# Performance work log

Measured on AMD Instinct MI355X. Metric: run time of the kernel, lower is better.

## Reference

```python
import jax, jax.numpy as jnp
import numpy as np

N, E = 10000, 160000
B, F, P, C = 16, 2, 12, 32


def gcn_norm(edge_index, edge_weight, n):
    # GCN symmetric normalization with self-loops (fill value 1.0, improved=False)
    src, dst = edge_index[0], edge_index[1]
    loop = jnp.arange(n, dtype=src.dtype)
    src = jnp.concatenate([src, loop])
    dst = jnp.concatenate([dst, loop])
    w = jnp.concatenate([edge_weight, jnp.ones((n,), edge_weight.dtype)])
    deg = jnp.zeros((n,), w.dtype).at[dst].add(w)
    dinv = jnp.where(deg > 0, jax.lax.rsqrt(deg), 0.0)
    return src, dst, dinv[src] * w * dinv[dst]


def gcn_conv(x, W, b, src, dst, norm, n):
    # x: [B, N, Fin] -> [B, N, Fout]; transform-then-propagate like GCNConv
    xw = x @ W
    msgs = xw[:, src, :] * norm[None, :, None]  # gather over source nodes
    out = jnp.zeros((x.shape[0], n, W.shape[1]), x.dtype).at[:, dst].add(msgs)
    return out + b


def setup_inputs():
    key = jax.random.key(0)
    ks = jax.random.split(key, 20)
    s = 0.1
    return {
        "x": jax.random.normal(ks[0], (B, N, F, P), jnp.float32),
        "edge_index": jax.random.randint(ks[1], (2, E), 0, N, jnp.int32),
        "edge_weight": jax.random.uniform(ks[2], (E,), jnp.float32),
        "W_z": jax.random.normal(ks[3], (F, C), jnp.float32) * s,
        "b_z": jnp.zeros((C,), jnp.float32),
        "lin_z_W": jax.random.normal(ks[4], (2 * C, C), jnp.float32) * s,
        "lin_z_b": jnp.zeros((C,), jnp.float32),
        "W_r": jax.random.normal(ks[5], (F, C), jnp.float32) * s,
        "b_r": jnp.zeros((C,), jnp.float32),
        "lin_r_W": jax.random.normal(ks[6], (2 * C, C), jnp.float32) * s,
        "lin_r_b": jnp.zeros((C,), jnp.float32),
        "W_h": jax.random.normal(ks[7], (F, C), jnp.float32) * s,
        "b_h": jnp.zeros((C,), jnp.float32),
        "lin_h_W": jax.random.normal(ks[8], (2 * C, C), jnp.float32) * s,
        "lin_h_b": jnp.zeros((C,), jnp.float32),
        "attention": jax.random.uniform(ks[9], (P,), jnp.float32),
        "lin_out_W": jax.random.normal(ks[10], (C, P), jnp.float32) * s,
        "lin_out_b": jnp.zeros((P,), jnp.float32),
    }


def reference(x, edge_index, edge_weight, W_z, b_z, lin_z_W, lin_z_b, W_r, b_r,
              lin_r_W, lin_r_b, W_h, b_h, lin_h_W, lin_h_b, attention,
              lin_out_W, lin_out_b):
    b, n, f, p = x.shape
    c = W_z.shape[1]
    src, dst, norm = gcn_norm(edge_index, edge_weight, n)
    probs = jax.nn.softmax(attention)  # attention over periods
    H0 = jnp.zeros((b, n, c), x.dtype)  # A3TGCN2 passes H=None each period
    xs = jnp.moveaxis(x, 3, 0)  # [P, B, N, F]

    def step(acc, inp):
        xp, w = inp  # xp: [B, N, F]
        Gz = gcn_conv(xp, W_z, b_z, src, dst, norm, n)
        Z = jax.nn.sigmoid(jnp.concatenate([Gz, H0], -1) @ lin_z_W + lin_z_b)
        Gr = gcn_conv(xp, W_r, b_r, src, dst, norm, n)
        R = jax.nn.sigmoid(jnp.concatenate([Gr, H0], -1) @ lin_r_W + lin_r_b)
        Gh = gcn_conv(xp, W_h, b_h, src, dst, norm, n)
        Ht = jnp.tanh(jnp.concatenate([Gh, H0 * R], -1) @ lin_h_W + lin_h_b)
        Hn = Z * H0 + (1.0 - Z) * Ht  # one GRU step from zero hidden
        return acc + w * Hn, None

    H_acc, _ = jax.lax.scan(step, H0, (xs, probs))
    h = jax.nn.relu(H_acc)
    return h @ lin_out_W + lin_out_b  # [B, N, periods]
```

## Files before the change

### kernel.cpp

```cpp
#include <hip/hip_runtime.h>
#include <hip/hip_bf16.h>

#define NN 10000
#define EE 160000
#define BB 16
#define PP 12
#define CC 32
#define XTOT (BB*NN*24)

__device__ __forceinline__ float fast_rcp(float x){ return __builtin_amdgcn_rcpf(x); }
__device__ __forceinline__ float fast_exp2(float x){
#if __has_builtin(__builtin_amdgcn_exp2f)
    return __builtin_amdgcn_exp2f(x);
#else
    return exp2f(x);
#endif
}
__device__ __forceinline__ unsigned short f2bfu(float f){
    union { float f; unsigned int i; } c; c.f = f;
    unsigned int r = c.i + 0x7FFFu + ((c.i >> 16) & 1u);
    return (unsigned short)(r >> 16);
}
__device__ __forceinline__ void up2(unsigned int u, float& a, float& b){
    union { unsigned int i; float f; } c;
    c.i = u << 16;          a = c.f;
    c.i = u & 0xFFFF0000u;  b = c.f;
}
__device__ __forceinline__ void unp24(uint4 q0, uint4 q1, uint4 q2, float* f){
    up2(q0.x,f[0],f[1]);   up2(q0.y,f[2],f[3]);   up2(q0.z,f[4],f[5]);   up2(q0.w,f[6],f[7]);
    up2(q1.x,f[8],f[9]);   up2(q1.y,f[10],f[11]); up2(q1.z,f[12],f[13]); up2(q1.w,f[14],f[15]);
    up2(q2.x,f[16],f[17]); up2(q2.y,f[18],f[19]); up2(q2.z,f[20],f[21]); up2(q2.w,f[22],f[23]);
}

__global__ __launch_bounds__(256) void k_stage(const float* __restrict__ x,
        const float* __restrict__ ew, const int* __restrict__ dst,
        unsigned short* __restrict__ xc, float* __restrict__ deg, int* __restrict__ cnt,
        const float* __restrict__ Wz, const float* __restrict__ bz,
        const float* __restrict__ LzW, const float* __restrict__ lzb,
        const float* __restrict__ Wh, const float* __restrict__ bh,
        const float* __restrict__ LhW, const float* __restrict__ lhb,
        const float* __restrict__ att, const float* __restrict__ LoW,
        const float* __restrict__ lob, float* __restrict__ wbuf){
    const float L2E = 1.4426950408889634f;
    int blk = blockIdx.x, tid = threadIdx.x;
    if (blk < 3750){
        int t  = blk*256 + tid;
        int o0 = t*4;
        int n  = o0 / 384;
        int j  = o0 - n*384;
        int b  = j / 24;
        int fp = j - b*24;
        float4 f = *(const float4*)(x + b*(NN*24) + n*24 + fp);
        ushort4 r; r.x=f2bfu(f.x); r.y=f2bfu(f.y); r.z=f2bfu(f.z); r.w=f2bfu(f.w);
        *(ushort4*)(xc + o0) = r;
        if (blk < 625){
            int e = blk*256 + tid;
            int d = dst[e];
            atomicAdd(&deg[d], ew[e]);
            atomicAdd(&cnt[d], 1);
        }
    } else {
        int c = tid;
        if (c < CC){
            float s0=0.f,s1=0.f,sb=lzb[c], h0=0.f,h1=0.f,hb=lhb[c];
            for (int k=0;k<CC;k++){
                float wz = LzW[k*CC+c];
                s0 += Wz[k]*wz; s1 += Wz[CC+k]*wz; sb += bz[k]*wz;
                float wh = LhW[k*CC+c];
                h0 += Wh[k]*wh; h1 += Wh[CC+k]*wh; hb += bh[k]*wh;
            }
            float* wp = wbuf + c*8;
            wp[0]=s0*L2E; wp[1]=s1*L2E; wp[2]=sb*L2E;
            wp[3]=h0*(2.f*L2E); wp[4]=h1*(2.f*L2E); wp[5]=hb*(2.f*L2E);
            wp[6]=0.f; wp[7]=0.f;
            for (int q=0;q<PP;q++) wbuf[288 + c*PP + q] = LoW[c*PP+q];
        } else if (c == 32){
            float a[PP]; float m = -1e30f;
            for (int p=0;p<PP;p++){ a[p]=att[p]; m = fmaxf(m, a[p]); }
            float s=0.f;
            for (int p=0;p<PP;p++){ a[p]=__expf(a[p]-m); s += a[p]; }
            float r = 1.f/s;
            for (int p=0;p<PP;p++) wbuf[256+p] = a[p]*r;
        } else if (c == 33){
            for (int q=0;q<PP;q++) wbuf[268+q] = lob[q];
        }
    }
}

__global__ __launch_bounds__(1024) void k_scan(const int* __restrict__ cnt,
        int* __restrict__ rowp, int* __restrict__ nxt){
    __shared__ int sums[1024];
    int tid = threadIdx.x;
    int lo = tid*10, hi = lo+10;
    if (lo > NN) lo = NN;
    if (hi > NN) hi = NN;
    int s = 0;
    for (int j=lo;j<hi;j++) s += cnt[j];
    sums[tid] = s;
    __syncthreads();
    for (int off=1; off<1024; off<<=1){
        int t = (tid >= off) ? sums[tid-off] : 0;
        __syncthreads();
        sums[tid] += t;
        __syncthreads();
    }
    int run = sums[tid] - s;
    if (tid == 0) rowp[0] = 0;
    for (int j=lo;j<hi;j++){
        nxt[j] = run;
        run += cnt[j];
        rowp[j+1] = run;
    }
}

__global__ __launch_bounds__(256) void k_scatter(const int* __restrict__ src,
        const int* __restrict__ dst, const float* __restrict__ ew,
        const float* __restrict__ deg, int* __restrict__ nxt,
        int* __restrict__ col, float* __restrict__ val){
    int e = blockIdx.x*256 + threadIdx.x;
    int s = src[e], d = dst[e];
    float v = rsqrtf(deg[s]+1.0f) * ew[e] * rsqrtf(deg[d]+1.0f);
    int pos = atomicAdd(&nxt[d], 1);
    col[pos] = s;
    val[pos] = v;
}

__global__ __launch_bounds__(128) void k_fused(const unsigned short* __restrict__ xc,
        const int* __restrict__ rowp, const int* __restrict__ col,
        const float* __restrict__ val, const float* __restrict__ deg,
        const float* __restrict__ wbuf, float* __restrict__ out){
    int tid = threadIdx.x;
    int g = tid >> 5, h = (tid >> 4) & 1, l = tid & 15;
    int n = blockIdx.x*4 + g;
    int e0 = rowp[n], e1 = rowp[n+1];

    float acc[24];
    #pragma unroll
    for (int k=0;k<24;k++) acc[k] = 0.f;
    const unsigned short* xl = xc + l*24;

    int e = e0 + h;
    for (; e + 2 < e1; e += 4){
        int s1 = col[e],  s2 = col[e+2];
        float v1 = val[e], v2 = val[e+2];
        const uint4* p1 = (const uint4*)(xl + s1*384);
        const uint4* p2 = (const uint4*)(xl + s2*384);
        uint4 qa0=p1[0], qa1=p1[1], qa2=p1[2];
        uint4 qb0=p2[0], qb1=p2[1], qb2=p2[2];
        float fa[24], fb[24];
        unp24(qa0,qa1,qa2,fa);
        unp24(qb0,qb1,qb2,fb);
        #pragma unroll
        for (int k=0;k<24;k++) acc[k] = fmaf(v1, fa[k], fmaf(v2, fb[k], acc[k]));
    }
    if (e < e1){
        int s1 = col[e];
        float v1 = val[e];
        const uint4* p1 = (const uint4*)(xl + s1*384);
        uint4 qa0=p1[0], qa1=p1[1], qa2=p1[2];
        float fa[24];
        unp24(qa0,qa1,qa2,fa);
        #pragma unroll
        for (int k=0;k<24;k++) acc[k] = fmaf(v1, fa[k], acc[k]);
    }
    if (h == 0){
        float v = fast_rcp(deg[n] + 1.0f);
        const uint4* p1 = (const uint4*)(xl + n*384);
        uint4 qa0=p1[0], qa1=p1[1], qa2=p1[2];
        float fa[24];
        unp24(qa0,qa1,qa2,fa);
        #pragma unroll
        for (int k=0;k<24;k++) acc[k] = fmaf(v, fa[k], acc[k]);
    }
    #pragma unroll
    for (int k=0;k<24;k++) acc[k] += __shfl_xor(acc[k], 16, 64);

    float pr[12];
    #pragma unroll
    for (int p=0;p<12;p++) pr[p] = wbuf[256+p];
    float o[12];
    #pragma unroll
    for (int q=0;q<12;q++) o[q] = 0.f;

    const float4* wp = (const float4*)wbuf;
    int cbase = h*16;
    for (int cc=0; cc<16; ++cc){
        int c = cbase + cc;
        float4 wa = wp[c*2];
        float4 wb = wp[c*2+1];
        float a = 0.f;
        #pragma unroll
        for (int p=0;p<12;p++){
            float y0 = acc[p], y1 = acc[12+p];
            float zs = fmaf(y1, wa.y, fmaf(y0, wa.x, wa.z));
            float hs = fmaf(y1, wb.x, fmaf(y0, wa.w, wb.y));
            zs = fminf(zs, 80.f); hs = fminf(hs, 80.f);
            float ez = fast_exp2(zs);
            float eh = fast_exp2(hs);
            float t  = fast_rcp((1.f+ez)*(1.f+eh));
            a = fmaf(pr[p]*(eh-1.f), t, a);
        }
        a = fmaxf(a, 0.f);
        const float4* lw = (const float4*)(wbuf + 288 + c*12);
        float4 w0 = lw[0], w1 = lw[1], w2 = lw[2];
        o[0]=fmaf(a,w0.x,o[0]); o[1]=fmaf(a,w0.y,o[1]); o[2] =fmaf(a,w0.z,o[2]);  o[3] =fmaf(a,w0.w,o[3]);
        o[4]=fmaf(a,w1.x,o[4]); o[5]=fmaf(a,w1.y,o[5]); o[6] =fmaf(a,w1.z,o[6]);  o[7] =fmaf(a,w1.w,o[7]);
        o[8]=fmaf(a,w2.x,o[8]); o[9]=fmaf(a,w2.y,o[9]); o[10]=fmaf(a,w2.z,o[10]); o[11]=fmaf(a,w2.w,o[11]);
    }
    #pragma unroll
    for (int q=0;q<12;q++) o[q] += __shfl_xor(o[q], 16, 64);
    if (h == 0){
        #pragma unroll
        for (int q=0;q<12;q++) o[q] += wbuf[268+q];
        float4* op = (float4*)(out + (l*NN + n)*12);
        op[0] = make_float4(o[0],o[1],o[2],o[3]);
        op[1] = make_float4(o[4],o[5],o[6],o[7]);
        op[2] = make_float4(o[8],o[9],o[10],o[11]);
    }
}

extern "C" void kernel_launch(void* const* d_in, const int* in_sizes, int n_in,
                              void* d_out, int out_size, void* d_ws, size_t ws_size,
                              hipStream_t stream) {
    const float* x   = (const float*)d_in[0];
    const int*   ei  = (const int*)d_in[1];
    const float* ew  = (const float*)d_in[2];
    const float* Wz  = (const float*)d_in[3];
    const float* bz  = (const float*)d_in[4];
    const float* LzW = (const float*)d_in[5];
    const float* lzb = (const float*)d_in[6];
    const float* Wh  = (const float*)d_in[11];
    const float* bh  = (const float*)d_in[12];
    const float* LhW = (const float*)d_in[13];
    const float* lhb = (const float*)d_in[14];
    const float* att = (const float*)d_in[15];
    const float* LoW = (const float*)d_in[16];
    const float* lob = (const float*)d_in[17];
    float* out = (float*)d_out;

    const int* srcI = ei;
    const int* dstI = ei + EE;

    char* ws = (char*)d_ws;
    size_t off = 0;
    auto alloc = [&](size_t bytes){ void* p = ws + off; off += (bytes + 255)/256*256; return p; };
    int*            degcnt = (int*)alloc(2*NN*4);
    float*          wbuf   = (float*)alloc(672*4);
    unsigned short* xc     = (unsigned short*)alloc((size_t)XTOT*2);
    int*            rowp   = (int*)alloc((NN+1)*4);
    int*            nxt    = (int*)alloc(NN*4);
    int*            col    = (int*)alloc(EE*4);
    float*          val    = (float*)alloc(EE*4);
    float* deg = (float*)degcnt;
    int*   cnt = degcnt + NN;

    hipMemsetAsync(degcnt, 0, 2*NN*4, stream);
    hipLaunchKernelGGL(k_stage,   dim3(3751), dim3(256),  0, stream,
                       x, ew, dstI, xc, deg, cnt,
                       Wz, bz, LzW, lzb, Wh, bh, LhW, lhb, att, LoW, lob, wbuf);
    hipLaunchKernelGGL(k_scan,    dim3(1),    dim3(1024), 0, stream, cnt, rowp, nxt);
    hipLaunchKernelGGL(k_scatter, dim3(EE/256), dim3(256), 0, stream,
                       srcI, dstI, ew, deg, nxt, col, val);
    hipLaunchKernelGGL(k_fused,   dim3(NN/4), dim3(128),  0, stream,
                       xc, rowp, col, val, deg, wbuf, out);
}
```

Measured before the change: 189.3 us.

## Merge all stages into one persistent kernel with software grid barriers

Replaces the memset plus four kernel launches with a single persistent kernel of 1024 blocks that moves between phases using atomic-counter grid barriers. Degree zeroing, staging, a two-level parallel prefix scan (in place of the single-block scan), CSR scatter and the fused gather/GRU/output stage all run inside it. The gather now uses one 64-lane wave per node and splits the channel loop over four lane groups. It also drops the clamp on the z exponent and expands the denominator. The aim is to remove launch gaps and the serial scan, at the cost of relying on all blocks being co-resident and of spin-wait barrier overhead.

```diff
diff --git a/kernel.cpp b/kernel.cpp
--- a/kernel.cpp
+++ b/kernel.cpp
@@ -7,6 +7,9 @@
 #define PP 12
 #define CC 32
 #define XTOT (BB*NN*24)
+#define NBLK 1024
+#define NTHR 128
+#define NT (NBLK*NTHR)
 
 __device__ __forceinline__ float fast_rcp(float x){ return __builtin_amdgcn_rcpf(x); }
 __device__ __forceinline__ float fast_exp2(float x){
@@ -32,34 +35,41 @@
     up2(q2.x,f[16],f[17]); up2(q2.y,f[18],f[19]); up2(q2.z,f[20],f[21]); up2(q2.w,f[22],f[23]);
 }
 
-__global__ __launch_bounds__(256) void k_stage(const float* __restrict__ x,
-        const float* __restrict__ ew, const int* __restrict__ dst,
-        unsigned short* __restrict__ xc, float* __restrict__ deg, int* __restrict__ cnt,
-        const float* __restrict__ Wz, const float* __restrict__ bz,
-        const float* __restrict__ LzW, const float* __restrict__ lzb,
-        const float* __restrict__ Wh, const float* __restrict__ bh,
-        const float* __restrict__ LhW, const float* __restrict__ lhb,
-        const float* __restrict__ att, const float* __restrict__ LoW,
-        const float* __restrict__ lob, float* __restrict__ wbuf){
-    const float L2E = 1.4426950408889634f;
-    int blk = blockIdx.x, tid = threadIdx.x;
-    if (blk < 3750){
-        int t  = blk*256 + tid;
-        int o0 = t*4;
-        int n  = o0 / 384;
-        int j  = o0 - n*384;
-        int b  = j / 24;
-        int fp = j - b*24;
-        float4 f = *(const float4*)(x + b*(NN*24) + n*24 + fp);
-        ushort4 r; r.x=f2bfu(f.x); r.y=f2bfu(f.y); r.z=f2bfu(f.z); r.w=f2bfu(f.w);
-        *(ushort4*)(xc + o0) = r;
-        if (blk < 625){
-            int e = blk*256 + tid;
-            int d = dst[e];
-            atomicAdd(&deg[d], ew[e]);
-            atomicAdd(&cnt[d], 1);
-        }
-    } else {
+__device__ __forceinline__ void gbar(int* bar, int idx){
+    __syncthreads();
+    if (threadIdx.x == 0){
+        __threadfence();
+        __hip_atomic_fetch_add(&bar[idx], 1, __ATOMIC_ACQ_REL, __HIP_MEMORY_SCOPE_AGENT);
+        while (__hip_atomic_load(&bar[idx], __ATOMIC_ACQUIRE, __HIP_MEMORY_SCOPE_AGENT) < NBLK){
+            __builtin_amdgcn_s_sleep(2);
+        }
+    }
+    __syncthreads();
+}
+
+__global__ __launch_bounds__(128, 4) void k_mega(
+    const float* __restrict__ x, const int* __restrict__ srcI, const int* __restrict__ dstI,
+    const float* __restrict__ ew,
+    const float* __restrict__ Wz, const float* __restrict__ bz,
+    const float* __restrict__ LzW, const float* __restrict__ lzb,
+    const float* __restrict__ Wh, const float* __restrict__ bh,
+    const float* __restrict__ LhW, const float* __restrict__ lhb,
+    const float* __restrict__ att, const float* __restrict__ LoW, const float* __restrict__ lob,
+    float* __restrict__ deg, int* __restrict__ cnt, float* __restrict__ wbuf,
+    unsigned short* __restrict__ xc, int* __restrict__ rowp, int* __restrict__ nxt,
+    int* __restrict__ col, float* __restrict__ val,
+    int* __restrict__ tmp, int* __restrict__ partial, int* __restrict__ bar,
+    float* __restrict__ out)
+{
+    const int tid = threadIdx.x, bid = blockIdx.x;
+    const int gid = bid*NTHR + tid;
+    __shared__ int shw[2];
+
+    if (gid < NN){ deg[gid] = 0.f; cnt[gid] = 0; }
+    gbar(bar, 0);
+
+    if (bid == NBLK-1){
+        const float L2E = 1.4426950408889634f;
         int c = tid;
         if (c < CC){
             float s0=0.f,s1=0.f,sb=lzb[c], h0=0.f,h1=0.f,hb=lhb[c];
@@ -85,137 +95,174 @@
             for (int q=0;q<PP;q++) wbuf[268+q] = lob[q];
         }
     }
-}
-
-__global__ __launch_bounds__(1024) void k_scan(const int* __restrict__ cnt,
-        int* __restrict__ rowp, int* __restrict__ nxt){
-    __shared__ int sums[1024];
-    int tid = threadIdx.x;
-    int lo = tid*10, hi = lo+10;
-    if (lo > NN) lo = NN;
-    if (hi > NN) hi = NN;
-    int s = 0;
-    for (int j=lo;j<hi;j++) s += cnt[j];
-    sums[tid] = s;
-    __syncthreads();
-    for (int off=1; off<1024; off<<=1){
-        int t = (tid >= off) ? sums[tid-off] : 0;
+    for (int t = gid; t < XTOT/4; t += NT){
+        int o0 = t*4;
+        int n  = o0 / 384;
+        int j  = o0 - n*384;
+        int b  = j / 24;
+        int fp = j - b*24;
+        float4 f = *(const float4*)(x + b*(NN*24) + n*24 + fp);
+        ushort4 r; r.x=f2bfu(f.x); r.y=f2bfu(f.y); r.z=f2bfu(f.z); r.w=f2bfu(f.w);
+        *(ushort4*)(xc + o0) = r;
+    }
+    for (int e = gid; e < EE; e += NT){
+        int d = dstI[e];
+        atomicAdd(&deg[d], ew[e]);
+        atomicAdd(&cnt[d], 1);
+    }
+    gbar(bar, 1);
+
+    {
+        int c = (gid < NN) ? cnt[gid] : 0;
+        int v = c;
+        #pragma unroll
+        for (int off=1; off<64; off<<=1){
+            int u = __shfl_up(v, off, 64);
+            if ((tid & 63) >= off) v += u;
+        }
+        if (tid == 63) shw[0] = v;
         __syncthreads();
-        sums[tid] += t;
+        int incl = v + ((tid >= 64) ? shw[0] : 0);
+        if (gid < NN) tmp[gid] = incl - c;
+        if (tid == NTHR-1) partial[bid] = incl;
+    }
+    gbar(bar, 2);
+
+    if (bid == 0){
+        int base = tid*8;
+        int lv[8]; int s = 0;
+        #pragma unroll
+        for (int j=0;j<8;j++){ lv[j] = partial[base+j]; s += lv[j]; }
+        int v = s;
+        #pragma unroll
+        for (int off=1; off<64; off<<=1){
+            int u = __shfl_up(v, off, 64);
+            if ((tid & 63) >= off) v += u;
+        }
+        if (tid == 63) shw[1] = v;
         __syncthreads();
-    }
-    int run = sums[tid] - s;
-    if (tid == 0) rowp[0] = 0;
-    for (int j=lo;j<hi;j++){
-        nxt[j] = run;
-        run += cnt[j];
-        rowp[j+1] = run;
-    }
-}
-
-__global__ __launch_bounds__(256) void k_scatter(const int* __restrict__ src,
-        const int* __restrict__ dst, const float* __restrict__ ew,
-        const float* __restrict__ deg, int* __restrict__ nxt,
-        int* __restrict__ col, float* __restrict__ val){
-    int e = blockIdx.x*256 + threadIdx.x;
-    int s = src[e], d = dst[e];
-    float v = rsqrtf(deg[s]+1.0f) * ew[e] * rsqrtf(deg[d]+1.0f);
-    int pos = atomicAdd(&nxt[d], 1);
-    col[pos] = s;
-    val[pos] = v;
-}
-
-__global__ __launch_bounds__(128) void k_fused(const unsigned short* __restrict__ xc,
-        const int* __restrict__ rowp, const int* __restrict__ col,
-        const float* __restrict__ val, const float* __restrict__ deg,
-        const float* __restrict__ wbuf, float* __restrict__ out){
-    int tid = threadIdx.x;
-    int g = tid >> 5, h = (tid >> 4) & 1, l = tid & 15;
-    int n = blockIdx.x*4 + g;
-    int e0 = rowp[n], e1 = rowp[n+1];
-
-    float acc[24];
-    #pragma unroll
-    for (int k=0;k<24;k++) acc[k] = 0.f;
-    const unsigned short* xl = xc + l*24;
-
-    int e = e0 + h;
-    for (; e + 2 < e1; e += 4){
-        int s1 = col[e],  s2 = col[e+2];
-        float v1 = val[e], v2 = val[e+2];
-        const uint4* p1 = (const uint4*)(xl + s1*384);
-        const uint4* p2 = (const uint4*)(xl + s2*384);
-        uint4 qa0=p1[0], qa1=p1[1], qa2=p1[2];
-        uint4 qb0=p2[0], qb1=p2[1], qb2=p2[2];
-        float fa[24], fb[24];
-        unp24(qa0,qa1,qa2,fa);
-        unp24(qb0,qb1,qb2,fb);
-        #pragma unroll
-        for (int k=0;k<24;k++) acc[k] = fmaf(v1, fa[k], fmaf(v2, fb[k], acc[k]));
-    }
-    if (e < e1){
-        int s1 = col[e];
-        float v1 = val[e];
-        const uint4* p1 = (const uint4*)(xl + s1*384);
-        uint4 qa0=p1[0], qa1=p1[1], qa2=p1[2];
-        float fa[24];
-        unp24(qa0,qa1,qa2,fa);
-        #pragma unroll
-        for (int k=0;k<24;k++) acc[k] = fmaf(v1, fa[k], acc[k]);
-    }
-    if (h == 0){
-        float v = fast_rcp(deg[n] + 1.0f);
-        const uint4* p1 = (const uint4*)(xl + n*384);
-        uint4 qa0=p1[0], qa1=p1[1], qa2=p1[2];
-        float fa[24];
-        unp24(qa0,qa1,qa2,fa);
-        #pragma unroll
-        for (int k=0;k<24;k++) acc[k] = fmaf(v, fa[k], acc[k]);
-    }
-    #pragma unroll
-    for (int k=0;k<24;k++) acc[k] += __shfl_xor(acc[k], 16, 64);
-
-    float pr[12];
-    #pragma unroll
-    for (int p=0;p<12;p++) pr[p] = wbuf[256+p];
-    float o[12];
-    #pragma unroll
-    for (int q=0;q<12;q++) o[q] = 0.f;
-
-    const float4* wp = (const float4*)wbuf;
-    int cbase = h*16;
-    for (int cc=0; cc<16; ++cc){
-        int c = cbase + cc;
-        float4 wa = wp[c*2];
-        float4 wb = wp[c*2+1];
-        float a = 0.f;
-        #pragma unroll
-        for (int p=0;p<12;p++){
-            float y0 = acc[p], y1 = acc[12+p];
-            float zs = fmaf(y1, wa.y, fmaf(y0, wa.x, wa.z));
-            float hs = fmaf(y1, wb.x, fmaf(y0, wa.w, wb.y));
-            zs = fminf(zs, 80.f); hs = fminf(hs, 80.f);
-            float ez = fast_exp2(zs);
-            float eh = fast_exp2(hs);
-            float t  = fast_rcp((1.f+ez)*(1.f+eh));
-            a = fmaf(pr[p]*(eh-1.f), t, a);
-        }
-        a = fmaxf(a, 0.f);
-        const float4* lw = (const float4*)(wbuf + 288 + c*12);
-        float4 w0 = lw[0], w1 = lw[1], w2 = lw[2];
-        o[0]=fmaf(a,w0.x,o[0]); o[1]=fmaf(a,w0.y,o[1]); o[2] =fmaf(a,w0.z,o[2]);  o[3] =fmaf(a,w0.w,o[3]);
-        o[4]=fmaf(a,w1.x,o[4]); o[5]=fmaf(a,w1.y,o[5]); o[6] =fmaf(a,w1.z,o[6]);  o[7] =fmaf(a,w1.w,o[7]);
-        o[8]=fmaf(a,w2.x,o[8]); o[9]=fmaf(a,w2.y,o[9]); o[10]=fmaf(a,w2.z,o[10]); o[11]=fmaf(a,w2.w,o[11]);
-    }
-    #pragma unroll
-    for (int q=0;q<12;q++) o[q] += __shfl_xor(o[q], 16, 64);
-    if (h == 0){
-        #pragma unroll
-        for (int q=0;q<12;q++) o[q] += wbuf[268+q];
-        float4* op = (float4*)(out + (l*NN + n)*12);
-        op[0] = make_float4(o[0],o[1],o[2],o[3]);
-        op[1] = make_float4(o[4],o[5],o[6],o[7]);
-        op[2] = make_float4(o[8],o[9],o[10],o[11]);
+        int incl = v + ((tid >= 64) ? shw[1] : 0);
+        int run = incl - s;
+        #pragma unroll
+        for (int j=0;j<8;j++){ int t2 = lv[j]; partial[base+j] = run; run += t2; }
+    }
+    gbar(bar, 3);
+
+    if (gid < NN){
+        int off = partial[bid] + tmp[gid];
+        rowp[gid] = off;
+        nxt[gid]  = off;
+    }
+    if (gid == 0) rowp[NN] = EE;
+    gbar(bar, 4);
+
+    for (int e = gid; e < EE; e += NT){
+        int s = srcI[e], d = dstI[e];
+        float v = rsqrtf(deg[s]+1.0f) * ew[e] * rsqrtf(deg[d]+1.0f);
+        int pos = atomicAdd(&nxt[d], 1);
+        col[pos] = s;
+        val[pos] = v;
+    }
+    gbar(bar, 5);
+
+    {
+        int lane = tid & 63;
+        int wv   = tid >> 6;
+        int h    = lane >> 4;
+        int l    = lane & 15;
+        const unsigned short* xl = xc + l*24;
+
+        float pr[12];
+        #pragma unroll
+        for (int p=0;p<12;p++) pr[p] = wbuf[256+p];
+
+        for (int n = bid*2 + wv; n < NN; n += NBLK*2){
+            int e0 = rowp[n], e1 = rowp[n+1];
+            float acc[24];
+            #pragma unroll
+            for (int k=0;k<24;k++) acc[k] = 0.f;
+
+            int e = e0 + h;
+            for (; e + 4 < e1; e += 8){
+                int s1 = col[e],  s2 = col[e+4];
+                float v1 = val[e], v2 = val[e+4];
+                const uint4* p1 = (const uint4*)(xl + s1*384);
+                const uint4* p2 = (const uint4*)(xl + s2*384);
+                uint4 qa0=p1[0], qa1=p1[1], qa2=p1[2];
+                uint4 qb0=p2[0], qb1=p2[1], qb2=p2[2];
+                float fa[24], fb[24];
+                unp24(qa0,qa1,qa2,fa);
+                unp24(qb0,qb1,qb2,fb);
+                #pragma unroll
+                for (int k=0;k<24;k++) acc[k] = fmaf(v1, fa[k], fmaf(v2, fb[k], acc[k]));
+            }
+            if (e < e1){
+                int s1 = col[e];
+                float v1 = val[e];
+                const uint4* p1 = (const uint4*)(xl + s1*384);
+                uint4 qa0=p1[0], qa1=p1[1], qa2=p1[2];
+                float fa[24];
+                unp24(qa0,qa1,qa2,fa);
+                #pragma unroll
+                for (int k=0;k<24;k++) acc[k] = fmaf(v1, fa[k], acc[k]);
+            }
+            if (h == 0){
+                float v = fast_rcp(deg[n] + 1.0f);
+                const uint4* p1 = (const uint4*)(xl + n*384);
+                uint4 qa0=p1[0], qa1=p1[1], qa2=p1[2];
+                float fa[24];
+                unp24(qa0,qa1,qa2,fa);
+                #pragma unroll
+                for (int k=0;k<24;k++) acc[k] = fmaf(v, fa[k], acc[k]);
+            }
+            #pragma unroll
+            for (int k=0;k<24;k++) acc[k] += __shfl_xor(acc[k], 16, 64);
+            #pragma unroll
+            for (int k=0;k<24;k++) acc[k] += __shfl_xor(acc[k], 32, 64);
+
+            float o[12];
+            #pragma unroll
+            for (int q=0;q<12;q++) o[q] = 0.f;
+            const float4* wp = (const float4*)wbuf;
+            int cbase = h*8;
+            #pragma unroll
+            for (int cc=0; cc<8; ++cc){
+                int c = cbase + cc;
+                float4 wa = wp[c*2];
+                float4 wb = wp[c*2+1];
+                float a = 0.f;
+                #pragma unroll
+                for (int p=0;p<12;p++){
+                    float y0 = acc[p], y1 = acc[12+p];
+                    float zs = fmaf(y1, wa.y, fmaf(y0, wa.x, wa.z));
+                    float hs = fmaf(y1, wb.x, fmaf(y0, wa.w, wb.y));
+                    hs = fminf(hs, 80.f);
+                    float ez = fast_exp2(zs);
+                    float eh = fast_exp2(hs);
+                    float den = fmaf(ez, eh, ez) + (eh + 1.f);
+                    float t  = fast_rcp(den);
+                    a = fmaf(pr[p]*(eh-1.f), t, a);
+                }
+                a = fmaxf(a, 0.f);
+                const float4* lw = (const float4*)(wbuf + 288 + c*12);
+                float4 w0 = lw[0], w1 = lw[1], w2 = lw[2];
+                o[0]=fmaf(a,w0.x,o[0]); o[1]=fmaf(a,w0.y,o[1]); o[2] =fmaf(a,w0.z,o[2]);  o[3] =fmaf(a,w0.w,o[3]);
+                o[4]=fmaf(a,w1.x,o[4]); o[5]=fmaf(a,w1.y,o[5]); o[6] =fmaf(a,w1.z,o[6]);  o[7] =fmaf(a,w1.w,o[7]);
+                o[8]=fmaf(a,w2.x,o[8]); o[9]=fmaf(a,w2.y,o[9]); o[10]=fmaf(a,w2.z,o[10]); o[11]=fmaf(a,w2.w,o[11]);
+            }
+            #pragma unroll
+            for (int q=0;q<12;q++) o[q] += __shfl_xor(o[q], 16, 64);
+            #pragma unroll
+            for (int q=0;q<12;q++) o[q] += __shfl_xor(o[q], 32, 64);
+            if (h == 0){
+                #pragma unroll
+                for (int q=0;q<12;q++) o[q] += wbuf[268+q];
+                float4* op = (float4*)(out + (l*NN + n)*12);
+                op[0] = make_float4(o[0],o[1],o[2],o[3]);
+                op[1] = make_float4(o[4],o[5],o[6],o[7]);
+                op[2] = make_float4(o[8],o[9],o[10],o[11]);
+            }
+        }
     }
 }
 
@@ -244,23 +291,22 @@
     char* ws = (char*)d_ws;
     size_t off = 0;
     auto alloc = [&](size_t bytes){ void* p = ws + off; off += (bytes + 255)/256*256; return p; };
-    int*            degcnt = (int*)alloc(2*NN*4);
-    float*          wbuf   = (float*)alloc(672*4);
-    unsigned short* xc     = (unsigned short*)alloc((size_t)XTOT*2);
-    int*            rowp   = (int*)alloc((NN+1)*4);
-    int*            nxt    = (int*)alloc(NN*4);
-    int*            col    = (int*)alloc(EE*4);
-    float*          val    = (float*)alloc(EE*4);
-    float* deg = (float*)degcnt;
-    int*   cnt = degcnt + NN;
-
-    hipMemsetAsync(degcnt, 0, 2*NN*4, stream);
-    hipLaunchKernelGGL(k_stage,   dim3(3751), dim3(256),  0, stream,
-                       x, ew, dstI, xc, deg, cnt,
-                       Wz, bz, LzW, lzb, Wh, bh, LhW, lhb, att, LoW, lob, wbuf);
-    hipLaunchKernelGGL(k_scan,    dim3(1),    dim3(1024), 0, stream, cnt, rowp, nxt);
-    hipLaunchKernelGGL(k_scatter, dim3(EE/256), dim3(256), 0, stream,
-                       srcI, dstI, ew, deg, nxt, col, val);
-    hipLaunchKernelGGL(k_fused,   dim3(NN/4), dim3(128),  0, stream,
-                       xc, rowp, col, val, deg, wbuf, out);
-}
+    int*            bar     = (int*)alloc(8*4);
+    float*          deg     = (float*)alloc(NN*4);
+    int*            cnt     = (int*)alloc(NN*4);
+    float*          wbuf    = (float*)alloc(672*4);
+    unsigned short* xc      = (unsigned short*)alloc((size_t)XTOT*2);
+    int*            rowp    = (int*)alloc((NN+1)*4);
+    int*            nxt     = (int*)alloc(NN*4);
+    int*            col     = (int*)alloc(EE*4);
+    float*          val     = (float*)alloc(EE*4);
+    int*            tmp     = (int*)alloc(NN*4);
+    int*            partial = (int*)alloc(NBLK*4);
+
+    hipMemsetAsync(bar, 0, 8*4, stream);
+    hipLaunchKernelGGL(k_mega, dim3(NBLK), dim3(NTHR), 0, stream,
+                       x, srcI, dstI, ew,
+                       Wz, bz, LzW, lzb, Wh, bh, LhW, lhb, att, LoW, lob,
+                       deg, cnt, wbuf, xc, rowp, nxt, col, val,
+                       tmp, partial, bar, out);
+}
```

Measured after the change: 644.8 us. 3.41x slower.
